# Optimization experiments

Measured on AMD Instinct MI355X. Metric: run time of the kernel, lower is better.

The kernel has to match this reference:

```python
import jax, jax.numpy as jnp
import numpy as np

B, T, I, H, O = 4096, 200, 2, 64, 2


def setup_inputs() -> dict:
    key = jax.random.key(0)
    ks = jax.random.split(key, 7)
    s = 1.0 / np.sqrt(H)  # PyTorch LSTM init scale
    return {
        "x": jax.random.normal(ks[0], (B, T, I), dtype=jnp.float32),
        "W_ih": jax.random.uniform(ks[1], (4 * H, I), jnp.float32, -s, s),
        "W_hh": jax.random.uniform(ks[2], (4 * H, H), jnp.float32, -s, s),
        "b_ih": jax.random.uniform(ks[3], (4 * H,), jnp.float32, -s, s),
        "b_hh": jax.random.uniform(ks[4], (4 * H,), jnp.float32, -s, s),
        "W_fc": jax.random.uniform(ks[5], (O, H), jnp.float32, -s, s),
        "b_fc": jax.random.uniform(ks[6], (O,), jnp.float32, -s, s),
    }


def reference(x, W_ih, W_hh, b_ih, b_hh, W_fc, b_fc):
    # Precompute input-to-gate projections for all timesteps in one GEMM.
    # xg: [T, B, 4H] (time-major for scan)
    xg = jnp.einsum("bti,gi->tbg", x, W_ih) + (b_ih + b_hh)

    def step(carry, xt):
        h, c = carry  # [B, H] each
        gates = xt + h @ W_hh.T  # [B, 4H]
        i_g, f_g, g_g, o_g = jnp.split(gates, 4, axis=-1)  # PyTorch order: i, f, g, o
        i = jax.nn.sigmoid(i_g)
        f = jax.nn.sigmoid(f_g)
        g = jnp.tanh(g_g)
        o = jax.nn.sigmoid(o_g)
        c = f * c + i * g
        h = o * jnp.tanh(c)
        return (h, c), None

    h0 = jnp.zeros((x.shape[0], W_hh.shape[1]), dtype=x.dtype)
    c0 = jnp.zeros_like(h0)
    (h_last, _), _ = jax.lax.scan(step, (h0, c0), xg)
    return h_last @ W_fc.T + b_fc  # [B, O]
```

## Files before the change

### kernel.cpp

```cpp
#include <hip/hip_runtime.h>
#include <hip/hip_bf16.h>


#define B_ 4096
#define T_ 200

typedef _Float16 half8 __attribute__((ext_vector_type(8)));
typedef float f32x4 __attribute__((ext_vector_type(4)));

#define K1f 1.4426950408889634f
#define K2f 2.8853900817779268f

__global__ __launch_bounds__(256) void lstm_kernel(
    const float* __restrict__ x,
    const float* __restrict__ W_ih,
    const float* __restrict__ W_hh,
    const float* __restrict__ b_ih,
    const float* __restrict__ b_hh,
    const float* __restrict__ W_fc,
    const float* __restrict__ b_fc,
    float* __restrict__ out)
{
    __shared__ float xs[16][404];
    __shared__ _Float16 h16[2][16][72];
    __shared__ float wfc[130];

    const int tid  = threadIdx.x;
    const int lane = tid & 63;
    const int w    = tid >> 6;
    const int cidx = lane & 15;
    const int grp  = lane >> 4;
    const int r0   = blockIdx.x * 16;

    for (int i4 = tid; i4 < 1600; i4 += 256) {
        const int row = i4 / 100;
        const int j4  = i4 - row * 100;
        reinterpret_cast<float4*>(&xs[row][0])[j4] =
            reinterpret_cast<const float4*>(x + (size_t)(r0 + row) * 400)[j4];
    }
    for (int i = tid; i < 1152; i += 256)
        reinterpret_cast<unsigned int*>(&h16[0][0][0])[i] = 0u;
    if (tid < 130) wfc[tid] = (tid < 128) ? W_fc[tid] : b_fc[tid - 128];

    half8 bfrag[4][2];
    float wi0[4], wi1[4], bs[4];
    const int u = w * 16 + cidx;
    #pragma unroll
    for (int m = 0; m < 4; ++m) {
        const float sc = (m == 2) ? K2f : -K1f;
        const int g = m * 64 + u;
        wi0[m] = W_ih[g * 2 + 0] * sc;
        wi1[m] = W_ih[g * 2 + 1] * sc;
        bs[m]  = (b_ih[g] + b_hh[g]) * sc;
        #pragma unroll
        for (int kt = 0; kt < 2; ++kt) {
            const float* p = W_hh + g * 64 + kt * 32 + grp * 8;
            const float4 lo = reinterpret_cast<const float4*>(p)[0];
            const float4 hi = reinterpret_cast<const float4*>(p)[1];
            half8 f;
            f[0] = (_Float16)(lo.x * sc); f[1] = (_Float16)(lo.y * sc);
            f[2] = (_Float16)(lo.z * sc); f[3] = (_Float16)(lo.w * sc);
            f[4] = (_Float16)(hi.x * sc); f[5] = (_Float16)(hi.y * sc);
            f[6] = (_Float16)(hi.z * sc); f[7] = (_Float16)(hi.w * sc);
            bfrag[m][kt] = f;
        }
    }

    float cst[4] = {0.f, 0.f, 0.f, 0.f};

    __syncthreads();

    for (int t = 0; t < T_; ++t) {
        const int rd = t & 1;
        const _Float16* hb = &h16[rd][0][0];
        const half8 a0 = *reinterpret_cast<const half8*>(hb + cidx * 72 + grp * 8);
        const half8 a1 = *reinterpret_cast<const half8*>(hb + cidx * 72 + 32 + grp * 8);

        float2 xv[4];
        #pragma unroll
        for (int r = 0; r < 4; ++r)
            xv[r] = *reinterpret_cast<const float2*>(&xs[grp * 4 + r][2 * t]);

        f32x4 acc[4];
        #pragma unroll
        for (int m = 0; m < 4; ++m) {
            f32x4 a = {fmaf(xv[0].y, wi1[m], fmaf(xv[0].x, wi0[m], bs[m])),
                       fmaf(xv[1].y, wi1[m], fmaf(xv[1].x, wi0[m], bs[m])),
                       fmaf(xv[2].y, wi1[m], fmaf(xv[2].x, wi0[m], bs[m])),
                       fmaf(xv[3].y, wi1[m], fmaf(xv[3].x, wi0[m], bs[m]))};
            a = __builtin_amdgcn_mfma_f32_16x16x32_f16(a0, bfrag[m][0], a, 0, 0, 0);
            a = __builtin_amdgcn_mfma_f32_16x16x32_f16(a1, bfrag[m][1], a, 0, 0, 0);
            acc[m] = a;
        }

        #pragma unroll
        for (int r = 0; r < 4; ++r) {
            const float Ei = __builtin_amdgcn_exp2f(acc[0][r]);
            const float Ef = __builtin_amdgcn_exp2f(acc[1][r]);
            const float Eg = __builtin_amdgcn_exp2f(acc[2][r]);
            const float Eo = __builtin_amdgcn_exp2f(acc[3][r]);

            const float fEf = 1.0f + Ef;
            const float P   = (1.0f + Ei) * (Eg + 1.0f);
            const float r1  = __builtin_amdgcn_rcpf(P * fEf);
            const float cv  = fmaf(cst[r], P, (Eg - 1.0f) * fEf) * r1;
            cst[r] = cv;

            const float Ec = __builtin_amdgcn_exp2f(fminf(K2f * cv, 60.0f));
            const float r2 = __builtin_amdgcn_rcpf((1.0f + Eo) * (Ec + 1.0f));
            const float hv = (Ec - 1.0f) * r2;

            h16[rd ^ 1][grp * 4 + r][u] = (_Float16)hv;
        }
        __syncthreads();
    }

    if (tid < 32) {
        const int r = tid & 15;
        const int o = tid >> 4;
        float s = wfc[128 + o];
        #pragma unroll
        for (int k = 0; k < 64; ++k)
            s = fmaf(wfc[o * 64 + k], (float)h16[0][r][k], s);
        out[(size_t)(r0 + r) * 2 + o] = s;
    }
}

extern "C" void kernel_launch(void* const* d_in, const int* in_sizes, int n_in,
                              void* d_out, int out_size, void* d_ws, size_t ws_size,
                              hipStream_t stream) {
    const float* x    = (const float*)d_in[0];
    const float* W_ih = (const float*)d_in[1];
    const float* W_hh = (const float*)d_in[2];
    const float* b_ih = (const float*)d_in[3];
    const float* b_hh = (const float*)d_in[4];
    const float* W_fc = (const float*)d_in[5];
    const float* b_fc = (const float*)d_in[6];
    float* out = (float*)d_out;

    lstm_kernel<<<B_ / 16, 256, 0, stream>>>(x, W_ih, W_hh, b_ih, b_hh, W_fc, b_fc, out);
}
```

Baseline: 127.0 us.

## Split each 16-row block's gate activations across two wave halves with 512 threads

```diff
diff --git a/kernel.cpp b/kernel.cpp
--- a/kernel.cpp
+++ b/kernel.cpp
@@ -11,7 +11,7 @@
 #define K1f 1.4426950408889634f
 #define K2f 2.8853900817779268f
 
-__global__ __launch_bounds__(256) void lstm_kernel(
+__global__ __launch_bounds__(512) void lstm_kernel(
     const float* __restrict__ x,
     const float* __restrict__ W_ih,
     const float* __restrict__ W_hh,
@@ -28,23 +28,25 @@
     const int tid  = threadIdx.x;
     const int lane = tid & 63;
     const int w    = tid >> 6;
+    const int wq   = w & 3;
+    const int half = w >> 2;
     const int cidx = lane & 15;
     const int grp  = lane >> 4;
     const int r0   = blockIdx.x * 16;
 
-    for (int i4 = tid; i4 < 1600; i4 += 256) {
+    for (int i4 = tid; i4 < 1600; i4 += 512) {
         const int row = i4 / 100;
         const int j4  = i4 - row * 100;
         reinterpret_cast<float4*>(&xs[row][0])[j4] =
             reinterpret_cast<const float4*>(x + (size_t)(r0 + row) * 400)[j4];
     }
-    for (int i = tid; i < 1152; i += 256)
+    for (int i = tid; i < 1152; i += 512)
         reinterpret_cast<unsigned int*>(&h16[0][0][0])[i] = 0u;
     if (tid < 130) wfc[tid] = (tid < 128) ? W_fc[tid] : b_fc[tid - 128];
 
     half8 bfrag[4][2];
     float wi0[4], wi1[4], bs[4];
-    const int u = w * 16 + cidx;
+    const int u = wq * 16 + cidx;
     #pragma unroll
     for (int m = 0; m < 4; ++m) {
         const float sc = (m == 2) ? K2f : -K1f;
@@ -66,9 +68,25 @@
         }
     }
 
-    float cst[4] = {0.f, 0.f, 0.f, 0.f};
+    const int rowA = grp * 4 + 2 * half;
+    float cstA = 0.f, cstB = 0.f;
 
     __syncthreads();
+
+    #define ACT(pi, pf, pg, po, cst, hvout)                                    \
+        {                                                                      \
+            const float Ei = __builtin_amdgcn_exp2f(pi);                       \
+            const float Ef = __builtin_amdgcn_exp2f(pf);                       \
+            const float Eg = __builtin_amdgcn_exp2f(pg);                       \
+            const float Eo = __builtin_amdgcn_exp2f(po);                       \
+            const float fEf = 1.0f + Ef;                                       \
+            const float P   = (1.0f + Ei) * (Eg + 1.0f);                       \
+            const float r1  = __builtin_amdgcn_rcpf(P * fEf);                  \
+            cst = fmaf(cst, P, (Eg - 1.0f) * fEf) * r1;                        \
+            const float Ec = __builtin_amdgcn_exp2f(fminf(K2f * cst, 60.0f));  \
+            const float r2 = __builtin_amdgcn_rcpf((1.0f + Eo) * (Ec + 1.0f)); \
+            hvout = (Ec - 1.0f) * r2;                                          \
+        }
 
     for (int t = 0; t < T_; ++t) {
         const int rd = t & 1;
@@ -76,42 +94,47 @@
         const half8 a0 = *reinterpret_cast<const half8*>(hb + cidx * 72 + grp * 8);
         const half8 a1 = *reinterpret_cast<const half8*>(hb + cidx * 72 + 32 + grp * 8);
 
-        float2 xv[4];
-        #pragma unroll
-        for (int r = 0; r < 4; ++r)
-            xv[r] = *reinterpret_cast<const float2*>(&xs[grp * 4 + r][2 * t]);
+        const float2 xvA = *reinterpret_cast<const float2*>(&xs[rowA][2 * t]);
+        const float2 xvB = *reinterpret_cast<const float2*>(&xs[rowA + 1][2 * t]);
 
-        f32x4 acc[4];
+        f32x4 Cin[4];
+        float pA[4], pB[4];
         #pragma unroll
         for (int m = 0; m < 4; ++m) {
-            f32x4 a = {fmaf(xv[0].y, wi1[m], fmaf(xv[0].x, wi0[m], bs[m])),
-                       fmaf(xv[1].y, wi1[m], fmaf(xv[1].x, wi0[m], bs[m])),
-                       fmaf(xv[2].y, wi1[m], fmaf(xv[2].x, wi0[m], bs[m])),
-                       fmaf(xv[3].y, wi1[m], fmaf(xv[3].x, wi0[m], bs[m]))};
-            a = __builtin_amdgcn_mfma_f32_16x16x32_f16(a0, bfrag[m][0], a, 0, 0, 0);
-            a = __builtin_amdgcn_mfma_f32_16x16x32_f16(a1, bfrag[m][1], a, 0, 0, 0);
-            acc[m] = a;
+            pA[m] = fmaf(xvA.y, wi1[m], fmaf(xvA.x, wi0[m], bs[m]));
+            pB[m] = fmaf(xvB.y, wi1[m], fmaf(xvB.x, wi0[m], bs[m]));
+        }
+        if (half == 0) {
+            #pragma unroll
+            for (int m = 0; m < 4; ++m) Cin[m] = (f32x4){pA[m], pB[m], 0.f, 0.f};
+        } else {
+            #pragma unroll
+            for (int m = 0; m < 4; ++m) Cin[m] = (f32x4){0.f, 0.f, pA[m], pB[m]};
         }
 
+        f32x4 lo[4], hi[4];
+        const f32x4 zero = {0.f, 0.f, 0.f, 0.f};
         #pragma unroll
-        for (int r = 0; r < 4; ++r) {
-            const float Ei = __builtin_amdgcn_exp2f(acc[0][r]);
-            const float Ef = __builtin_amdgcn_exp2f(acc[1][r]);
-            const float Eg = __builtin_amdgcn_exp2f(acc[2][r]);
-            const float Eo = __builtin_amdgcn_exp2f(acc[3][r]);
+        for (int m = 0; m < 4; ++m) {
+            lo[m] = __builtin_amdgcn_mfma_f32_16x16x32_f16(a0, bfrag[m][0], Cin[m], 0, 0, 0);
+            hi[m] = __builtin_amdgcn_mfma_f32_16x16x32_f16(a1, bfrag[m][1], zero, 0, 0, 0);
+        }
 
-            const float fEf = 1.0f + Ef;
-            const float P   = (1.0f + Ei) * (Eg + 1.0f);
-            const float r1  = __builtin_amdgcn_rcpf(P * fEf);
-            const float cv  = fmaf(cst[r], P, (Eg - 1.0f) * fEf) * r1;
-            cst[r] = cv;
+        float hvA, hvB;
+        if (half == 0) {
+            ACT(lo[0][0] + hi[0][0], lo[1][0] + hi[1][0], lo[2][0] + hi[2][0],
+                lo[3][0] + hi[3][0], cstA, hvA);
+            ACT(lo[0][1] + hi[0][1], lo[1][1] + hi[1][1], lo[2][1] + hi[2][1],
+                lo[3][1] + hi[3][1], cstB, hvB);
+        } else {
+            ACT(lo[0][2] + hi[0][2], lo[1][2] + hi[1][2], lo[2][2] + hi[2][2],
+                lo[3][2] + hi[3][2], cstA, hvA);
+            ACT(lo[0][3] + hi[0][3], lo[1][3] + hi[1][3], lo[2][3] + hi[2][3],
+                lo[3][3] + hi[3][3], cstB, hvB);
+        }
 
-            const float Ec = __builtin_amdgcn_exp2f(fminf(K2f * cv, 60.0f));
-            const float r2 = __builtin_amdgcn_rcpf((1.0f + Eo) * (Ec + 1.0f));
-            const float hv = (Ec - 1.0f) * r2;
-
-            h16[rd ^ 1][grp * 4 + r][u] = (_Float16)hv;
-        }
+        h16[rd ^ 1][rowA][u]     = (_Float16)hvA;
+        h16[rd ^ 1][rowA + 1][u] = (_Float16)hvB;
         __syncthreads();
     }
 
@@ -138,5 +161,5 @@
     const float* b_fc = (const float*)d_in[6];
     float* out = (float*)d_out;
 
-    lstm_kernel<<<B_ / 16, 256, 0, stream>>>(x, W_ih, W_hh, b_ih, b_hh, W_fc, b_fc, out);
+    lstm_kernel<<<B_ / 16, 512, 0, stream>>>(x, W_ih, W_hh, b_ih, b_hh, W_fc, b_fc, out);
 }
```

Result: slower. 146.8 us (+15.6%).

## Give each wavefront its own 4 batch rows to drop per-step block barriers

Applied to the files above, without the earlier changes.

```diff
diff --git a/kernel.cpp b/kernel.cpp
--- a/kernel.cpp
+++ b/kernel.cpp
@@ -11,7 +11,7 @@
 #define K1f 1.4426950408889634f
 #define K2f 2.8853900817779268f
 
-__global__ __launch_bounds__(256) void lstm_kernel(
+__global__ __launch_bounds__(256, 1) void lstm_kernel(
     const float* __restrict__ x,
     const float* __restrict__ W_ih,
     const float* __restrict__ W_hh,
@@ -22,14 +22,13 @@
     float* __restrict__ out)
 {
     __shared__ float xs[16][404];
-    __shared__ _Float16 h16[2][16][72];
-    __shared__ float wfc[130];
+    __shared__ _Float16 hsh[4][4][80];
 
     const int tid  = threadIdx.x;
     const int lane = tid & 63;
     const int w    = tid >> 6;
-    const int cidx = lane & 15;
-    const int grp  = lane >> 4;
+    const int c    = lane & 15;
+    const int g    = lane >> 4;
     const int r0   = blockIdx.x * 16;
 
     for (int i4 = tid; i4 < 1600; i4 += 256) {
@@ -38,23 +37,21 @@
         reinterpret_cast<float4*>(&xs[row][0])[j4] =
             reinterpret_cast<const float4*>(x + (size_t)(r0 + row) * 400)[j4];
     }
-    for (int i = tid; i < 1152; i += 256)
-        reinterpret_cast<unsigned int*>(&h16[0][0][0])[i] = 0u;
-    if (tid < 130) wfc[tid] = (tid < 128) ? W_fc[tid] : b_fc[tid - 128];
+    for (int i = tid; i < 640; i += 256)
+        reinterpret_cast<unsigned int*>(&hsh[0][0][0])[i] = 0u;
+    __syncthreads();
 
-    half8 bfrag[4][2];
-    float wi0[4], wi1[4], bs[4];
-    const int u = w * 16 + cidx;
+    half8 bfrag[16][2];
+    float cw0[16], cw1[16], cbs[16];
     #pragma unroll
-    for (int m = 0; m < 4; ++m) {
+    for (int j = 0; j < 16; ++j) {
+        const int m  = j & 3;
+        const int ub = j >> 2;
         const float sc = (m == 2) ? K2f : -K1f;
-        const int g = m * 64 + u;
-        wi0[m] = W_ih[g * 2 + 0] * sc;
-        wi1[m] = W_ih[g * 2 + 1] * sc;
-        bs[m]  = (b_ih[g] + b_hh[g]) * sc;
+        const int gr = 64 * m + 16 * ub + c;
         #pragma unroll
         for (int kt = 0; kt < 2; ++kt) {
-            const float* p = W_hh + g * 64 + kt * 32 + grp * 8;
+            const float* p = W_hh + gr * 64 + kt * 32 + g * 8;
             const float4 lo = reinterpret_cast<const float4*>(p)[0];
             const float4 hi = reinterpret_cast<const float4*>(p)[1];
             half8 f;
@@ -62,67 +59,74 @@
             f[2] = (_Float16)(lo.z * sc); f[3] = (_Float16)(lo.w * sc);
             f[4] = (_Float16)(hi.x * sc); f[5] = (_Float16)(hi.y * sc);
             f[6] = (_Float16)(hi.z * sc); f[7] = (_Float16)(hi.w * sc);
-            bfrag[m][kt] = f;
+            bfrag[j][kt] = f;
+        }
+        cw0[j] = W_ih[gr * 2 + 0] * sc;
+        cw1[j] = W_ih[gr * 2 + 1] * sc;
+        cbs[j] = (b_ih[gr] + b_hh[gr]) * sc;
+    }
+
+    const int arow = c >> 2;
+    const _Float16* hrd = &hsh[w][arow][0];
+    _Float16*       hwr = &hsh[w][g][0];
+
+    float cst[4] = {0.f, 0.f, 0.f, 0.f};
+    float hvk[4];
+
+    for (int t = 0; t < T_; ++t) {
+        const half8 a0 = *reinterpret_cast<const half8*>(hrd + g * 8);
+        const half8 a1 = *reinterpret_cast<const half8*>(hrd + 32 + g * 8);
+        const float2 xv = *reinterpret_cast<const float2*>(&xs[4 * w + g][2 * t]);
+
+        f32x4 acc[16];
+        #pragma unroll
+        for (int j = 0; j < 16; ++j) {
+            f32x4 z = {0.f, 0.f, 0.f, 0.f};
+            z = __builtin_amdgcn_mfma_f32_16x16x32_f16(a0, bfrag[j][0], z, 0, 0, 0);
+            z = __builtin_amdgcn_mfma_f32_16x16x32_f16(a1, bfrag[j][1], z, 0, 0, 0);
+            acc[j] = z;
+        }
+
+        #pragma unroll
+        for (int s = 0; s < 4; ++s) {
+            float pre[4];
+            #pragma unroll
+            for (int m = 0; m < 4; ++m) {
+                const int j = 4 * s + m;
+                pre[m] = fmaf(xv.y, cw1[j], fmaf(xv.x, cw0[j], cbs[j])) + acc[j][0];
+            }
+            const float Ei = __builtin_amdgcn_exp2f(pre[0]);
+            const float Ef = __builtin_amdgcn_exp2f(pre[1]);
+            const float Eg = __builtin_amdgcn_exp2f(pre[2]);
+            const float Eo = __builtin_amdgcn_exp2f(pre[3]);
+            const float fEf = 1.0f + Ef;
+            const float P   = (1.0f + Ei) * (Eg + 1.0f);
+            const float r1  = __builtin_amdgcn_rcpf(P * fEf);
+            const float cv  = fmaf(cst[s], P, (Eg - 1.0f) * fEf) * r1;
+            cst[s] = cv;
+            const float Ec = __builtin_amdgcn_exp2f(fminf(K2f * cv, 60.0f));
+            const float r2 = __builtin_amdgcn_rcpf((1.0f + Eo) * (Ec + 1.0f));
+            const float hv = (Ec - 1.0f) * r2;
+            hvk[s] = hv;
+            hwr[16 * s + c] = (_Float16)hv;
         }
     }
 
-    float cst[4] = {0.f, 0.f, 0.f, 0.f};
-
-    __syncthreads();
-
-    for (int t = 0; t < T_; ++t) {
-        const int rd = t & 1;
-        const _Float16* hb = &h16[rd][0][0];
-        const half8 a0 = *reinterpret_cast<const half8*>(hb + cidx * 72 + grp * 8);
-        const half8 a1 = *reinterpret_cast<const half8*>(hb + cidx * 72 + 32 + grp * 8);
-
-        float2 xv[4];
-        #pragma unroll
-        for (int r = 0; r < 4; ++r)
-            xv[r] = *reinterpret_cast<const float2*>(&xs[grp * 4 + r][2 * t]);
-
-        f32x4 acc[4];
-        #pragma unroll
-        for (int m = 0; m < 4; ++m) {
-            f32x4 a = {fmaf(xv[0].y, wi1[m], fmaf(xv[0].x, wi0[m], bs[m])),
-                       fmaf(xv[1].y, wi1[m], fmaf(xv[1].x, wi0[m], bs[m])),
-                       fmaf(xv[2].y, wi1[m], fmaf(xv[2].x, wi0[m], bs[m])),
-                       fmaf(xv[3].y, wi1[m], fmaf(xv[3].x, wi0[m], bs[m]))};
-            a = __builtin_amdgcn_mfma_f32_16x16x32_f16(a0, bfrag[m][0], a, 0, 0, 0);
-            a = __builtin_amdgcn_mfma_f32_16x16x32_f16(a1, bfrag[m][1], a, 0, 0, 0);
-            acc[m] = a;
-        }
-
-        #pragma unroll
-        for (int r = 0; r < 4; ++r) {
-            const float Ei = __builtin_amdgcn_exp2f(acc[0][r]);
-            const float Ef = __builtin_amdgcn_exp2f(acc[1][r]);
-            const float Eg = __builtin_amdgcn_exp2f(acc[2][r]);
-            const float Eo = __builtin_amdgcn_exp2f(acc[3][r]);
-
-            const float fEf = 1.0f + Ef;
-            const float P   = (1.0f + Ei) * (Eg + 1.0f);
-            const float r1  = __builtin_amdgcn_rcpf(P * fEf);
-            const float cv  = fmaf(cst[r], P, (Eg - 1.0f) * fEf) * r1;
-            cst[r] = cv;
-
-            const float Ec = __builtin_amdgcn_exp2f(fminf(K2f * cv, 60.0f));
-            const float r2 = __builtin_amdgcn_rcpf((1.0f + Eo) * (Ec + 1.0f));
-            const float hv = (Ec - 1.0f) * r2;
-
-            h16[rd ^ 1][grp * 4 + r][u] = (_Float16)hv;
-        }
-        __syncthreads();
+    float p0 = 0.f, p1 = 0.f;
+    #pragma unroll
+    for (int s = 0; s < 4; ++s) {
+        p0 = fmaf(W_fc[16 * s + c],      hvk[s], p0);
+        p1 = fmaf(W_fc[64 + 16 * s + c], hvk[s], p1);
     }
-
-    if (tid < 32) {
-        const int r = tid & 15;
-        const int o = tid >> 4;
-        float s = wfc[128 + o];
-        #pragma unroll
-        for (int k = 0; k < 64; ++k)
-            s = fmaf(wfc[o * 64 + k], (float)h16[0][r][k], s);
-        out[(size_t)(r0 + r) * 2 + o] = s;
+    #pragma unroll
+    for (int mk = 1; mk < 16; mk <<= 1) {
+        p0 += __shfl_xor(p0, mk);
+        p1 += __shfl_xor(p1, mk);
+    }
+    if (c == 0) {
+        const int row = r0 + 4 * w + g;
+        out[row * 2 + 0] = p0 + b_fc[0];
+        out[row * 2 + 1] = p1 + b_fc[1];
     }
 }
 
```

Measured after the change: 132.8 us. 1.05x slower.
